# Optimization experiments

Hardware: AMD Instinct MI355X
Metric: run time of the kernel (lower is better)

Reference implementation:

```python
import jax, jax.numpy as jnp
import numpy as np

B, S, D, H = 2, 2048, 2048, 16
HD = D // H  # head_dim = 128


def setup_inputs() -> dict:
    key = jax.random.key(0)
    k1, k2, k3, k4, k5, k6 = jax.random.split(key, 6)
    scale = 1.0 / np.sqrt(D)
    return {
        "hidden_states": jax.random.normal(k1, (B, S, D), dtype=jnp.float32),
        "attention_mask": jnp.ones((B, S), dtype=jnp.int32),
        "wq": jax.random.normal(k2, (D, D), dtype=jnp.float32) * scale,
        "wk": jax.random.normal(k3, (D, D), dtype=jnp.float32) * scale,
        "wv": jax.random.normal(k4, (D, D), dtype=jnp.float32) * scale,
        "wo": jax.random.normal(k5, (D, D), dtype=jnp.float32) * scale,
        "bo": jax.random.normal(k6, (D,), dtype=jnp.float32) * 0.01,
    }


def reference(hidden_states, attention_mask, wq, wk, wv, wo, bo):
    b, s, d = hidden_states.shape
    # QKV projections (no bias), split heads -> [B, S, H, HD]
    q = (hidden_states @ wq).reshape(b, s, H, HD)
    k = (hidden_states @ wk).reshape(b, s, H, HD)
    v = (hidden_states @ wv).reshape(b, s, H, HD)

    # combined causal + padding mask -> [B, 1, S, S]
    causal = jnp.tril(jnp.ones((s, s), dtype=bool))[None, None]
    pad = (attention_mask > 0)[:, None, None, :]  # [B,1,1,S]
    mask = jnp.logical_and(causal, pad)

    big_neg = jnp.finfo(hidden_states.dtype).min
    bias = jnp.where(mask, 0.0, big_neg).astype(hidden_states.dtype)

    # scaled dot-product attention (flax dot_product_attention scales by 1/sqrt(head_dim))
    scores = jnp.einsum("bqhd,bkhd->bhqk", q, k) / jnp.sqrt(jnp.asarray(HD, hidden_states.dtype))
    probs = jax.nn.softmax(scores + bias, axis=-1)
    ctx = jnp.einsum("bhqk,bkhd->bqhd", probs, v).reshape(b, s, d)

    return ctx @ wo + bo
```

## Files before the change

### kernel.cpp

```cpp
#include <hip/hip_runtime.h>
#include <hip/hip_bf16.h>
#include <stdint.h>

#define Bv 2
#define Sv 2048
#define Dv 2048
#define Hv 16
#define HDv 128
#define Mv (Bv*Sv)

typedef __attribute__((ext_vector_type(8))) short short8;
typedef __attribute__((ext_vector_type(4))) short short4v;
typedef __attribute__((ext_vector_type(4))) float f32x4;

__device__ __forceinline__ unsigned short bf16_rne(float f) {
    union { float f; uint32_t u; } c; c.f = f;
    uint32_t u = c.u;
    u += 0x7fffu + ((u >> 16) & 1u);
    return (unsigned short)(u >> 16);
}

__device__ __forceinline__ uint32_t cvt_pk_bf16(float lo, float hi) {
    uint32_t r;
    asm("v_cvt_pk_bf16_f32 %0, %1, %2" : "=v"(r) : "v"(lo), "v"(hi));
    return r;
}

__device__ __forceinline__ void gload16(const void* g, void* l) {
    __builtin_amdgcn_global_load_lds((const __attribute__((address_space(1))) void*)g,
                                     (__attribute__((address_space(3))) void*)l, 16, 0, 0);
}

#define BARRIER() asm volatile("s_barrier" ::: "memory")
#define LGKM0()   do { asm volatile("s_waitcnt lgkmcnt(0)" ::: "memory"); \
                       __builtin_amdgcn_sched_barrier(0); } while (0)

__global__ void cvt_x_kernel(const float* __restrict__ x, unsigned short* __restrict__ xb) {
    int i = (blockIdx.x * 256 + threadIdx.x) * 8;
    float4 v0 = *(const float4*)(x + i);
    float4 v1 = *(const float4*)(x + i + 4);
    short8 o;
    o[0] = (short)bf16_rne(v0.x); o[1] = (short)bf16_rne(v0.y);
    o[2] = (short)bf16_rne(v0.z); o[3] = (short)bf16_rne(v0.w);
    o[4] = (short)bf16_rne(v1.x); o[5] = (short)bf16_rne(v1.y);
    o[6] = (short)bf16_rne(v1.z); o[7] = (short)bf16_rne(v1.w);
    *(short8*)(xb + i) = o;
}

__global__ void cvt_wt_kernel(const float* __restrict__ w0, const float* __restrict__ w1,
                              const float* __restrict__ w2, const float* __restrict__ w3,
                              unsigned short* __restrict__ wt) {
    __shared__ unsigned short t[64 * 65];
    const int tid = threadIdx.x;
    int z = blockIdx.z;
    const float* w = (z == 0) ? w0 : (z == 1) ? w1 : (z == 2) ? w2 : w3;
    unsigned short* o = wt + (size_t)z * Dv * Dv;
    int k0 = blockIdx.x * 64, n0 = blockIdx.y * 64;
    #pragma unroll
    for (int j = 0; j < 4; ++j) {
        int r = (tid >> 4) + j * 16;
        int c = (tid & 15) * 4;
        float4 v = *(const float4*)&w[(size_t)(k0 + r) * Dv + n0 + c];
        t[r * 65 + c + 0] = bf16_rne(v.x);
        t[r * 65 + c + 1] = bf16_rne(v.y);
        t[r * 65 + c + 2] = bf16_rne(v.z);
        t[r * 65 + c + 3] = bf16_rne(v.w);
    }
    __syncthreads();
    #pragma unroll
    for (int j = 0; j < 2; ++j) {
        int flat = tid + j * 256;
        int nn = flat >> 3;
        int kk = (flat & 7) * 8;
        short8 v;
        #pragma unroll
        for (int e = 0; e < 8; ++e) v[e] = (short)t[(kk + e) * 65 + nn];
        *(short8*)&o[(size_t)(n0 + nn) * Dv + k0 + kk] = v;
    }
}

__global__ __launch_bounds__(512, 2) void gemm8ph_kernel(
    const unsigned short* __restrict__ A,
    const unsigned short* __restrict__ WtBase,
    unsigned short* __restrict__ CbBase)
{
    extern __shared__ unsigned short lds[];
    const int tid = threadIdx.x;
    const int wv = tid >> 6, ln = tid & 63;
    const int lr = ln & 15, lg = ln >> 4;
    const int wm = wv >> 2, wn = wv & 3;

    const int bid = blockIdx.x;
    const int xcd = bid & 7, idx = bid >> 3;
    const int n_idx = xcd * 2 + idx / 16;
    const int m_idx = idx % 16;
    const int m0 = m_idx * 256, n0g = n_idx * 256;

    const int lrow = wv * 8 + (ln >> 3);
    const int lcol = ((ln & 7) ^ (ln >> 3)) << 3;
    const unsigned short* Ag = A      + (size_t)(m0  + lrow) * Dv + lcol;
    const unsigned short* Bg = WtBase + (size_t)(n0g + lrow) * Dv + lcol;

    auto SH = [&](int T, int isB, int h) {
        const unsigned short* src = (isB ? Bg : Ag) + (size_t)(h * 128) * Dv + T * 64;
        unsigned short* dst = &lds[(T & 1) * 32768 + isB * 16384 + h * 8192 + wv * 512];
        gload16(src, dst);
        gload16(src + (size_t)64 * Dv, dst + 4096);
    };

    const int axk = lr & 7;
    auto RDA = [&](int buf, int fm, int ks) {
        return *(const short8*)&lds[buf * 32768 + (wm * 128 + fm * 16 + lr) * 64 + (((ks * 4 + lg) ^ axk) << 3)];
    };
    auto RDB = [&](int buf, int fn, int ks) {
        return *(const short8*)&lds[buf * 32768 + 16384 + (wn * 64 + fn * 16 + lr) * 64 + (((ks * 4 + lg) ^ axk) << 3)];
    };

    f32x4 acc[8][4];
    #pragma unroll
    for (int fm = 0; fm < 8; fm++)
        #pragma unroll
        for (int fn = 0; fn < 4; fn++)
            acc[fm][fn] = (f32x4){0.f, 0.f, 0.f, 0.f};

    SH(0, 0, 0); SH(0, 0, 1); SH(0, 1, 0); SH(0, 1, 1);
    SH(1, 1, 0); SH(1, 0, 0);
    asm volatile("s_waitcnt vmcnt(4)" ::: "memory");
    BARRIER();

    short8 af[8], b0[4], b1[4];
    const int NT2 = 16;

    #define MFMA_BLK(FN0, FN1, BARR) do {                                              \
        __builtin_amdgcn_s_setprio(1);                                                 \
        _Pragma("unroll")                                                              \
        for (int fm = 0; fm < 8; fm++) {                                               \
            acc[fm][FN0] = __builtin_amdgcn_mfma_f32_16x16x32_bf16(af[fm], BARR[FN0], acc[fm][FN0], 0, 0, 0); \
            acc[fm][FN1] = __builtin_amdgcn_mfma_f32_16x16x32_bf16(af[fm], BARR[FN1], acc[fm][FN1], 0, 0, 0); \
        }                                                                              \
        __builtin_amdgcn_s_setprio(0);                                                 \
    } while (0)

    for (int i = 0; i < NT2; ++i) {
        const int Tb = 2 * i + 1;
        const bool more = (i + 1 < NT2);

        #pragma unroll
        for (int fm = 0; fm < 8; fm++) af[fm] = RDA(0, fm, 0);
        #pragma unroll
        for (int fn = 0; fn < 4; fn++) b0[fn] = RDB(0, fn, 0);
        SH(Tb, 0, 1);
        BARRIER(); LGKM0();
        MFMA_BLK(0, 1, b0);
        BARRIER();

        #pragma unroll
        for (int fn = 0; fn < 4; fn++) b1[fn] = RDB(0, fn, 1);
        SH(Tb, 1, 1);
        BARRIER(); LGKM0();
        MFMA_BLK(2, 3, b0);
        BARRIER();

        #pragma unroll
        for (int fm = 0; fm < 8; fm++) af[fm] = RDA(0, fm, 1);
        if (more) SH(Tb + 1, 1, 0);
        BARRIER(); LGKM0();
        MFMA_BLK(0, 1, b1);
        BARRIER();

        if (more) SH(Tb + 1, 0, 0);
        BARRIER(); LGKM0();
        MFMA_BLK(2, 3, b1);
        if (more) asm volatile("s_waitcnt vmcnt(4)" ::: "memory");
        else      asm volatile("s_waitcnt vmcnt(0)" ::: "memory");
        BARRIER();

        #pragma unroll
        for (int fm = 0; fm < 8; fm++) af[fm] = RDA(1, fm, 0);
        #pragma unroll
        for (int fn = 0; fn < 4; fn++) b0[fn] = RDB(1, fn, 0);
        if (more) SH(Tb + 1, 0, 1);
        BARRIER(); LGKM0();
        MFMA_BLK(0, 1, b0);
        BARRIER();

        #pragma unroll
        for (int fn = 0; fn < 4; fn++) b1[fn] = RDB(1, fn, 1);
        if (more) SH(Tb + 1, 1, 1);
        BARRIER(); LGKM0();
        MFMA_BLK(2, 3, b0);
        BARRIER();

        #pragma unroll
        for (int fm = 0; fm < 8; fm++) af[fm] = RDA(1, fm, 1);
        if (more) SH(Tb + 2, 1, 0);
        BARRIER(); LGKM0();
        MFMA_BLK(0, 1, b1);
        BARRIER();

        if (more) SH(Tb + 2, 0, 0);
        BARRIER(); LGKM0();
        MFMA_BLK(2, 3, b1);
        if (more) {
            asm volatile("s_waitcnt vmcnt(4)" ::: "memory");
            BARRIER();
        }
    }
    #undef MFMA_BLK

    const int z = n0g >> 11;
    unsigned short* Cz = CbBase + (size_t)z * Mv * Dv;
    const int ncl = (n0g & 2047) + wn * 64;
    #pragma unroll
    for (int fm = 0; fm < 8; fm++)
        #pragma unroll
        for (int fn = 0; fn < 4; fn++) {
            int row = m0 + wm * 128 + fm * 16 + lg * 4;
            int col = ncl + fn * 16 + lr;
            #pragma unroll
            for (int r = 0; r < 4; r++)
                Cz[(size_t)(row + r) * Dv + col] = bf16_rne(acc[fm][fn][r]);
        }
}

template<int FOUT>
__global__ __launch_bounds__(512, 2) void gemm8_kernel(
    const unsigned short* __restrict__ A,
    const unsigned short* __restrict__ WtBase,
    unsigned short* __restrict__ Cb,
    float* __restrict__ Cf,
    const float* __restrict__ bias)
{
    extern __shared__ unsigned short lds[];
    const int tid = threadIdx.x;
    const int wv = tid >> 6, ln = tid & 63;
    const int lr = ln & 15, lg = ln >> 4;
    const int wm = wv >> 2, wn = wv & 3;

    const int bid = blockIdx.x;
    const int xcd = bid & 7, idx = bid >> 3;
    const int n_idx = xcd;
    const int m_idx = idx;
    const int m0 = m_idx * 128;
    const int n0g = n_idx * 256;
    const int NT = Dv / 64;

    const int srow = ln >> 3;
    const int swz = ((ln & 7) ^ srow) << 3;
    const unsigned short* Ab = A      + (size_t)(m0  + wv * 8 + srow) * Dv + swz;
    const unsigned short* Bb = WtBase + (size_t)(n0g + wv * 8 + srow) * Dv + swz;

    auto STAGE_A = [&](int t, int d) {
        const unsigned short* g = Ab + t * 64;
        #pragma unroll
        for (int j = 0; j < 2; ++j)
            gload16(g + (size_t)(j * 64) * Dv, &lds[d * 24576 + (j * 64 + wv * 8) * 64]);
    };
    auto STAGE_B = [&](int t, int d) {
        const unsigned short* g = Bb + t * 64;
        #pragma unroll
        for (int j = 0; j < 4; ++j)
            gload16(g + (size_t)(j * 64) * Dv, &lds[d * 24576 + 8192 + (j * 64 + wv * 8) * 64]);
    };

    const int aro = (wm * 64 + lr) * 64;
    const int bro = (wn * 64 + lr) * 64;
    const int ach0 = ((lg ^ (lr & 7)) << 3);
    const int ach1 = (((4 + lg) ^ (lr & 7)) << 3);

    f32x4 acc[4][4];
    #pragma unroll
    for (int mi = 0; mi < 4; mi++)
        #pragma unroll
        for (int ni = 0; ni < 4; ni++)
            acc[mi][ni] = (f32x4){0.f, 0.f, 0.f, 0.f};

    STAGE_A(0, 0); STAGE_B(0, 0);
    STAGE_A(1, 1); STAGE_B(1, 1);
    asm volatile("s_waitcnt vmcnt(6)" ::: "memory");
    BARRIER();

    for (int t = 0; t < NT; ++t) {
        const int d = t % 3, d2 = (t + 2) % 3;
        const unsigned short* la = &lds[d * 24576];
        const unsigned short* lb = &lds[d * 24576 + 8192];

        short8 af[4][2], bf0[2][2];
        #pragma unroll
        for (int mi = 0; mi < 4; mi++) {
            af[mi][0] = *(const short8*)&la[aro + mi * 1024 + ach0];
            af[mi][1] = *(const short8*)&la[aro + mi * 1024 + ach1];
        }
        #pragma unroll
        for (int ni = 0; ni < 2; ni++) {
            bf0[ni][0] = *(const short8*)&lb[bro + ni * 1024 + ach0];
            bf0[ni][1] = *(const short8*)&lb[bro + ni * 1024 + ach1];
        }
        if (t + 2 < NT) STAGE_A(t + 2, d2);
        BARRIER();
        __builtin_amdgcn_s_setprio(1);
        #pragma unroll
        for (int mi = 0; mi < 4; mi++)
            #pragma unroll
            for (int ni = 0; ni < 2; ni++) {
                acc[mi][ni] = __builtin_amdgcn_mfma_f32_16x16x32_bf16(af[mi][0], bf0[ni][0], acc[mi][ni], 0, 0, 0);
                acc[mi][ni] = __builtin_amdgcn_mfma_f32_16x16x32_bf16(af[mi][1], bf0[ni][1], acc[mi][ni], 0, 0, 0);
            }
        __builtin_amdgcn_s_setprio(0);

        short8 bf1[2][2];
        #pragma unroll
        for (int ni = 0; ni < 2; ni++) {
            bf1[ni][0] = *(const short8*)&lb[bro + (ni + 2) * 1024 + ach0];
            bf1[ni][1] = *(const short8*)&lb[bro + (ni + 2) * 1024 + ach1];
        }
        if (t + 2 < NT) STAGE_B(t + 2, d2);
        asm volatile("s_waitcnt vmcnt(6)" ::: "memory");
        BARRIER();
        __builtin_amdgcn_s_setprio(1);
        #pragma unroll
        for (int mi = 0; mi < 4; mi++)
            #pragma unroll
            for (int ni = 0; ni < 2; ni++) {
                acc[mi][ni + 2] = __builtin_amdgcn_mfma_f32_16x16x32_bf16(af[mi][0], bf1[ni][0], acc[mi][ni + 2], 0, 0, 0);
                acc[mi][ni + 2] = __builtin_amdgcn_mfma_f32_16x16x32_bf16(af[mi][1], bf1[ni][1], acc[mi][ni + 2], 0, 0, 0);
            }
        __builtin_amdgcn_s_setprio(0);
    }

    if (FOUT) {
        #pragma unroll
        for (int mi = 0; mi < 4; mi++)
            #pragma unroll
            for (int ni = 0; ni < 4; ni++) {
                int row = m0 + wm * 64 + mi * 16 + lg * 4;
                int col = n0g + wn * 64 + ni * 16 + lr;
                float bv = bias[col];
                #pragma unroll
                for (int r = 0; r < 4; r++)
                    Cf[(size_t)(row + r) * Dv + col] = acc[mi][ni][r] + bv;
            }
    } else {
        __syncthreads();
        unsigned short* T = lds;
        #pragma unroll
        for (int mi = 0; mi < 4; mi++)
            #pragma unroll
            for (int ni = 0; ni < 4; ni++) {
                int row = wm * 64 + mi * 16 + lg * 4;
                int col = wn * 64 + ni * 16 + lr;
                int cb = (row >> 2) ^ (col & 31);
                short4v o;
                #pragma unroll
                for (int r = 0; r < 4; r++) o[r] = (short)bf16_rne(acc[mi][ni][r]);
                *(short4v*)&T[col * 128 + cb * 4] = o;
            }
        __syncthreads();
        const int bb = m0 >> 11;
        const int s0 = m0 & 2047;
        unsigned short* VTb = Cb + (size_t)bb * Dv * Sv;
        #pragma unroll
        for (int j = 0; j < 8; ++j) {
            int flat = tid + j * 512;
            int col = flat >> 4;
            int s16 = flat & 15;
            int c5 = col & 31;
            short4v lo = *(const short4v*)&T[col * 128 + (((s16 * 2)     ^ c5) << 2)];
            short4v hi = *(const short4v*)&T[col * 128 + (((s16 * 2 + 1) ^ c5) << 2)];
            short8 v;
            v[0] = lo[0]; v[1] = lo[1]; v[2] = lo[2]; v[3] = lo[3];
            v[4] = hi[0]; v[5] = hi[1]; v[6] = hi[2]; v[7] = hi[3];
            *(short8*)&VTb[(size_t)(n0g + col) * Sv + s0 + s16 * 8] = v;
        }
    }
}

__global__ __launch_bounds__(512) void attn_kernel(
    const unsigned short* __restrict__ Q, const unsigned short* __restrict__ K,
    const unsigned short* __restrict__ VT, const int* __restrict__ pmask,
    unsigned short* __restrict__ CTX)
{
    __shared__ unsigned short lK[2][64 * 128];
    __shared__ unsigned short lVt[2][128 * 64];
    __shared__ int lPmB[2][64];
    __shared__ int lPmOk[2];

    const int tid = threadIdx.x, wv = tid >> 6, ln = tid & 63;
    const int lr = ln & 15, lg = ln >> 4;
    const int L = blockIdx.x;
    const int bh = (L & 7) * 4 + ((L >> 3) & 3);
    const int b = bh >> 4, h = bh & 15;
    const int v = L >> 5;
    const int qidx = (v < 8) ? (15 - v) : (v - 8);
    const int q0 = qidx * 128;
    const int qw0 = q0 + wv * 16;
    const size_t hoff  = (size_t)b * Sv * Dv + (size_t)h * HDv;
    const size_t vtoff = ((size_t)b * Dv + (size_t)h * HDv) * Sv;

    short8 qf[4];
    #pragma unroll
    for (int ds = 0; ds < 4; ds++)
        qf[ds] = *(const short8*)&Q[hoff + (size_t)(qw0 + lr) * Dv + ds * 32 + lg * 8];

    size_t koff[2], voff[2];
    #pragma unroll
    for (int ii = 0; ii < 2; ++ii) {
        int slot = ii * 512 + wv * 64 + ln;
        int krow = slot >> 4, kch = slot & 15;
        koff[ii] = hoff + (size_t)krow * Dv + ((kch ^ (krow & 7)) << 3);
        int vrow = slot >> 3, vch = slot & 7;
        voff[ii] = vtoff + (size_t)vrow * Sv + ((vch ^ (vrow & 7)) << 3);
    }

    auto STAGE = [&](int t, int buf) {
        const size_t kadd = (size_t)(t << 6) * Dv;
        const int vadd = t << 6;
        unsigned short* kb = &lK[buf][0];
        unsigned short* vb = &lVt[buf][0];
        #pragma unroll
        for (int ii = 0; ii < 2; ++ii) {
            gload16(K + koff[ii] + kadd, kb + (ii * 512 + wv * 64) * 8);
            gload16(VT + voff[ii] + vadd, vb + (ii * 512 + wv * 64) * 8);
        }
        if (wv == 0) {
            int pmv = pmask[b * Sv + (t << 6) + ln];
            lPmB[buf][ln] = pmv;
            unsigned long long bal = __ballot(pmv != 0);
            if (ln == 0) lPmOk[buf] = (bal == ~0ull) ? 1 : 0;
        }
    };

    f32x4 acc[8];
    #pragma unroll
    for (int n = 0; n < 8; n++) acc[n] = (f32x4){0.f, 0.f, 0.f, 0.f};
    float mrow = -3.0e38f, lrow = 0.f;
    const float CS = 0.12751744f;
    const int qg = qw0 + lr;
    const int nt = (q0 >> 6) + 2;
    const int srcA = lr + ((lg & 1) << 5);
    const int srcB = srcA + 16;
    const bool hiSel = (lg >= 2);

    auto TILE = [&](int t, int buf, auto CAUSAL_c) {
        constexpr bool CAUSAL = decltype(CAUSAL_c)::value;
        const int kv0 = t << 6;
        const unsigned short* kb = &lK[buf][0];
        const unsigned short* vb = &lVt[buf][0];

        f32x4 st[4];
        #pragma unroll
        for (int t2 = 0; t2 < 4; ++t2) st[t2] = (f32x4){0.f, 0.f, 0.f, 0.f};
        __builtin_amdgcn_s_setprio(1);
        #pragma unroll
        for (int t2 = 0; t2 < 4; ++t2) {
            const int krow = t2 * 16 + lr;
            #pragma unroll
            for (int ds = 0; ds < 4; ++ds) {
                const int ch = ds * 4 + lg;
                short8 kf = *(const short8*)&kb[krow * 128 + ((ch ^ (krow & 7)) << 3)];
                st[t2] = __builtin_amdgcn_mfma_f32_16x16x32_bf16(kf, qf[ds], st[t2], 0, 0, 0);
            }
        }
        __builtin_amdgcn_s_setprio(0);

        float sv[4][4];
        float rmax;
        if constexpr (CAUSAL) {
            const int* pm = &lPmB[buf][0];
            #pragma unroll
            for (int t2 = 0; t2 < 4; ++t2)
                #pragma unroll
                for (int r = 0; r < 4; ++r) {
                    int kvl = t2 * 16 + lg * 4 + r;
                    bool ok = ((kv0 + kvl) <= qg) && (pm[kvl] != 0);
                    sv[t2][r] = ok ? st[t2][r] * CS : -1.0e30f;
                }
            rmax = sv[0][0];
            #pragma unroll
            for (int t2 = 0; t2 < 4; ++t2)
                #pragma unroll
                for (int r = 0; r < 4; ++r) rmax = fmaxf(rmax, sv[t2][r]);
            rmax = fmaxf(rmax, __shfl_xor(rmax, 16, 64));
            rmax = fmaxf(rmax, __shfl_xor(rmax, 32, 64));
        } else {
            rmax = st[0][0];
            #pragma unroll
            for (int t2 = 0; t2 < 4; ++t2)
                #pragma unroll
                for (int r = 0; r < 4; ++r) rmax = fmaxf(rmax, st[t2][r]);
            rmax = fmaxf(rmax, __shfl_xor(rmax, 16, 64));
            rmax = fmaxf(rmax, __shfl_xor(rmax, 32, 64));
            rmax *= CS;
        }

        if (!__all(rmax - mrow <= 8.0f)) {
            float mn = fmaxf(mrow, rmax);
            float alpha = exp2f(mrow - mn);
            mrow = mn;
            lrow *= alpha;
            #pragma unroll
            for (int n = 0; n < 8; n++)
                #pragma unroll
                for (int r = 0; r < 4; r++) acc[n][r] *= alpha;
        }

        float p[4][4]; float psum = 0.f;
        if constexpr (CAUSAL) {
            #pragma unroll
            for (int t2 = 0; t2 < 4; ++t2)
                #pragma unroll
                for (int r = 0; r < 4; ++r) {
                    float e = exp2f(sv[t2][r] - mrow);
                    p[t2][r] = (sv[t2][r] > -5.0e29f) ? e : 0.f;
                    psum += p[t2][r];
                }
        } else {
            if (lPmOk[buf]) {
                #pragma unroll
                for (int t2 = 0; t2 < 4; ++t2)
                    #pragma unroll
                    for (int r = 0; r < 4; ++r) {
                        p[t2][r] = exp2f(fmaf(st[t2][r], CS, -mrow));
                        psum += p[t2][r];
                    }
            } else {
                const int* pm = &lPmB[buf][0];
                #pragma unroll
                for (int t2 = 0; t2 < 4; ++t2)
                    #pragma unroll
                    for (int r = 0; r < 4; ++r) {
                        int kvl = t2 * 16 + lg * 4 + r;
                        float e = exp2f(fmaf(st[t2][r], CS, -mrow));
                        p[t2][r] = (pm[kvl] != 0) ? e : 0.f;
                        psum += p[t2][r];
                    }
            }
        }
        psum += __shfl_xor(psum, 16, 64);
        psum += __shfl_xor(psum, 32, 64);
        lrow += psum;

        uint32_t pk[4][2];
        #pragma unroll
        for (int t2 = 0; t2 < 4; ++t2)
            #pragma unroll
            for (int pp = 0; pp < 2; ++pp)
                pk[t2][pp] = cvt_pk_bf16(p[t2][2 * pp], p[t2][2 * pp + 1]);

        union U { uint32_t u[4]; short8 s; } pa0, pa1;
        {
            uint32_t l0 = (uint32_t)__shfl((int)pk[0][0], srcA, 64), h0 = (uint32_t)__shfl((int)pk[1][0], srcA, 64);
            uint32_t l1 = (uint32_t)__shfl((int)pk[0][1], srcA, 64), h1 = (uint32_t)__shfl((int)pk[1][1], srcA, 64);
            uint32_t l2 = (uint32_t)__shfl((int)pk[0][0], srcB, 64), h2 = (uint32_t)__shfl((int)pk[1][0], srcB, 64);
            uint32_t l3 = (uint32_t)__shfl((int)pk[0][1], srcB, 64), h3 = (uint32_t)__shfl((int)pk[1][1], srcB, 64);
            pa0.u[0] = hiSel ? h0 : l0; pa0.u[1] = hiSel ? h1 : l1;
            pa0.u[2] = hiSel ? h2 : l2; pa0.u[3] = hiSel ? h3 : l3;
        }
        {
            uint32_t l0 = (uint32_t)__shfl((int)pk[2][0], srcA, 64), h0 = (uint32_t)__shfl((int)pk[3][0], srcA, 64);
            uint32_t l1 = (uint32_t)__shfl((int)pk[2][1], srcA, 64), h1 = (uint32_t)__shfl((int)pk[3][1], srcA, 64);
            uint32_t l2 = (uint32_t)__shfl((int)pk[2][0], srcB, 64), h2 = (uint32_t)__shfl((int)pk[3][0], srcB, 64);
            uint32_t l3 = (uint32_t)__shfl((int)pk[2][1], srcB, 64), h3 = (uint32_t)__shfl((int)pk[3][1], srcB, 64);
            pa1.u[0] = hiSel ? h0 : l0; pa1.u[1] = hiSel ? h1 : l1;
            pa1.u[2] = hiSel ? h2 : l2; pa1.u[3] = hiSel ? h3 : l3;
        }

        __builtin_amdgcn_s_setprio(1);
        #pragma unroll
        for (int n = 0; n < 8; n++) {
            const int vrow = n * 16 + lr;
            short8 a0 = *(const short8*)&vb[vrow * 64 + ((lg ^ (vrow & 7)) << 3)];
            acc[n] = __builtin_amdgcn_mfma_f32_16x16x32_bf16(a0, pa0.s, acc[n], 0, 0, 0);
            short8 a1 = *(const short8*)&vb[vrow * 64 + (((4 + lg) ^ (vrow & 7)) << 3)];
            acc[n] = __builtin_amdgcn_mfma_f32_16x16x32_bf16(a1, pa1.s, acc[n], 0, 0, 0);
        }
        __builtin_amdgcn_s_setprio(0);
    };

    STAGE(0, 0);
    __syncthreads();
    int cur = 0;

    for (int t = 0; t < nt; ++t) {
        if (t + 1 < nt) STAGE(t + 1, cur ^ 1);
        const int kv0 = t << 6;
        if (kv0 <= qw0 + 15) {
            if (kv0 + 63 > qw0) TILE(t, cur, std::integral_constant<bool, true>{});
            else                TILE(t, cur, std::integral_constant<bool, false>{});
        }
        __syncthreads();
        cur ^= 1;
    }

    float inv = 1.0f / lrow;
    #pragma unroll
    for (int n = 0; n < 8; n++) {
        short4v o;
        #pragma unroll
        for (int r = 0; r < 4; r++) o[r] = (short)bf16_rne(acc[n][r] * inv);
        *(short4v*)&CTX[hoff + (size_t)qg * Dv + n * 16 + lg * 4] = o;
    }
}

extern "C" void kernel_launch(void* const* d_in, const int* in_sizes, int n_in,
                              void* d_out, int out_size, void* d_ws, size_t ws_size,
                              hipStream_t stream) {
    const float* hs  = (const float*)d_in[0];
    const int*   am  = (const int*)d_in[1];
    const float* wq  = (const float*)d_in[2];
    const float* wk  = (const float*)d_in[3];
    const float* wv_ = (const float*)d_in[4];
    const float* wo  = (const float*)d_in[5];
    const float* bo  = (const float*)d_in[6];
    float* out = (float*)d_out;

    char* ws = (char*)d_ws;
    unsigned short* Xb  = (unsigned short*)ws;
    unsigned short* Wt  = (unsigned short*)(ws + (size_t)16 * 1024 * 1024);
    unsigned short* QKV = (unsigned short*)(ws + (size_t)48 * 1024 * 1024);
    unsigned short* CTX = (unsigned short*)(ws + (size_t)96 * 1024 * 1024);
    unsigned short* VT  = QKV + 2 * (size_t)Mv * Dv;

    const int LDSB_8PH = 131072;
    const int LDSB_R   = 147456;
    static bool attrSet = false;
    if (!attrSet) {
        hipFuncSetAttribute((const void*)gemm8ph_kernel, hipFuncAttributeMaxDynamicSharedMemorySize, LDSB_8PH);
        hipFuncSetAttribute((const void*)gemm8_kernel<0>, hipFuncAttributeMaxDynamicSharedMemorySize, LDSB_R);
        hipFuncSetAttribute((const void*)gemm8_kernel<1>, hipFuncAttributeMaxDynamicSharedMemorySize, LDSB_R);
        attrSet = true;
    }

    hipLaunchKernelGGL(cvt_x_kernel, dim3(Mv * Dv / 8 / 256), dim3(256), 0, stream, hs, Xb);
    hipLaunchKernelGGL(cvt_wt_kernel, dim3(32, 32, 4), dim3(256), 0, stream, wq, wk, wv_, wo, Wt);
    hipLaunchKernelGGL(gemm8ph_kernel, dim3(256), dim3(512), LDSB_8PH, stream, Xb, Wt, QKV);
    hipLaunchKernelGGL(gemm8_kernel<0>, dim3(256), dim3(512), LDSB_R, stream,
                       Xb, Wt + 2 * (size_t)Dv * Dv, VT, (float*)nullptr, (const float*)nullptr);
    hipLaunchKernelGGL(attn_kernel, dim3(512), dim3(512), 0, stream,
                       QKV, QKV + (size_t)Mv * Dv, VT, am, CTX);
    hipLaunchKernelGGL(gemm8_kernel<1>, dim3(256), dim3(512), LDSB_R, stream,
                       CTX, Wt + 3 * (size_t)Dv * Dv, (unsigned short*)nullptr, out, bo);
}
```

Before: 227.6 us.

## Split heavy causal query tiles across two KV halves and merge partial results

The eight heaviest causal query tiles per head are each split into two blocks that cover separate halves of the KV range. The grid grows from 512 to 768 blocks, which evens out work per block across the CUs. Each half writes an unnormalized bf16 partial output plus its row max and sum into workspace that reuses the already-consumed Wq/Wk/Wv weight buffers. A new merge kernel then rescales and combines the halves into CTX. The cost is an extra launch, extra global traffic for the partials, and bf16 rounding of the unnormalized partial accumulators.

```diff
diff --git a/kernel.cpp b/kernel.cpp
--- a/kernel.cpp
+++ b/kernel.cpp
@@ -18,6 +18,11 @@
     uint32_t u = c.u;
     u += 0x7fffu + ((u >> 16) & 1u);
     return (unsigned short)(u >> 16);
+}
+
+__device__ __forceinline__ float bf16_to_f(unsigned short s) {
+    union { uint32_t u; float f; } c; c.u = ((uint32_t)s) << 16;
+    return c.f;
 }
 
 __device__ __forceinline__ uint32_t cvt_pk_bf16(float lo, float hi) {
@@ -378,7 +383,8 @@
 __global__ __launch_bounds__(512) void attn_kernel(
     const unsigned short* __restrict__ Q, const unsigned short* __restrict__ K,
     const unsigned short* __restrict__ VT, const int* __restrict__ pmask,
-    unsigned short* __restrict__ CTX)
+    unsigned short* __restrict__ CTX,
+    unsigned short* __restrict__ PO, float* __restrict__ PML)
 {
     __shared__ unsigned short lK[2][64 * 128];
     __shared__ unsigned short lVt[2][128 * 64];
@@ -390,8 +396,22 @@
     const int L = blockIdx.x;
     const int bh = (L & 7) * 4 + ((L >> 3) & 3);
     const int b = bh >> 4, h = bh & 15;
-    const int v = L >> 5;
-    const int qidx = (v < 8) ? (15 - v) : (v - 8);
+    const int s = L >> 5;
+    int qidx, t0, t1, half = 0;
+    bool heavy;
+    if (s < 16) {
+        heavy = true;
+        qidx = 15 - (s >> 1);
+        half = s & 1;
+        int ht = qidx + 1;
+        t0 = half ? ht : 0;
+        t1 = half ? (2 * qidx + 2) : ht;
+    } else {
+        heavy = false;
+        qidx = 23 - s;
+        t0 = 0;
+        t1 = 2 * qidx + 2;
+    }
     const int q0 = qidx * 128;
     const int qw0 = q0 + wv * 16;
     const size_t hoff  = (size_t)b * Sv * Dv + (size_t)h * HDv;
@@ -436,7 +456,6 @@
     float mrow = -3.0e38f, lrow = 0.f;
     const float CS = 0.12751744f;
     const int qg = qw0 + lr;
-    const int nt = (q0 >> 6) + 2;
     const int srcA = lr + ((lg & 1) << 5);
     const int srcB = srcA + 16;
     const bool hiSel = (lg >= 2);
@@ -577,12 +596,12 @@
         __builtin_amdgcn_s_setprio(0);
     };
 
-    STAGE(0, 0);
+    STAGE(t0, 0);
     __syncthreads();
     int cur = 0;
 
-    for (int t = 0; t < nt; ++t) {
-        if (t + 1 < nt) STAGE(t + 1, cur ^ 1);
+    for (int t = t0; t < t1; ++t) {
+        if (t + 1 < t1) STAGE(t + 1, cur ^ 1);
         const int kv0 = t << 6;
         if (kv0 <= qw0 + 15) {
             if (kv0 + 63 > qw0) TILE(t, cur, std::integral_constant<bool, true>{});
@@ -592,13 +611,65 @@
         cur ^= 1;
     }
 
-    float inv = 1.0f / lrow;
-    #pragma unroll
-    for (int n = 0; n < 8; n++) {
-        short4v o;
-        #pragma unroll
-        for (int r = 0; r < 4; r++) o[r] = (short)bf16_rne(acc[n][r] * inv);
-        *(short4v*)&CTX[hoff + (size_t)qg * Dv + n * 16 + lg * 4] = o;
+    if (!heavy) {
+        float inv = 1.0f / lrow;
+        #pragma unroll
+        for (int n = 0; n < 8; n++) {
+            short4v o;
+            #pragma unroll
+            for (int r = 0; r < 4; r++) o[r] = (short)bf16_rne(acc[n][r] * inv);
+            *(short4v*)&CTX[hoff + (size_t)qg * Dv + n * 16 + lg * 4] = o;
+        }
+    } else {
+        const int qtl = qidx - 8;
+        const int ql = qg - q0;
+        const size_t base = ((size_t)(bh * 8 + qtl) * 2 + half) * 128 + ql;
+        #pragma unroll
+        for (int n = 0; n < 8; n++) {
+            short4v o;
+            #pragma unroll
+            for (int r = 0; r < 4; r++) o[r] = (short)bf16_rne(acc[n][r]);
+            *(short4v*)&PO[base * 128 + n * 16 + lg * 4] = o;
+        }
+        if (lg == 0) {
+            PML[base * 2]     = mrow;
+            PML[base * 2 + 1] = lrow;
+        }
+    }
+}
+
+__global__ __launch_bounds__(256) void merge_kernel(
+    const unsigned short* __restrict__ PO, const float* __restrict__ PML,
+    unsigned short* __restrict__ CTX)
+{
+    const int qt = blockIdx.x;
+    const int bh = blockIdx.y;
+    const int b = bh >> 4, h = bh & 15;
+    const size_t hoff = (size_t)b * Sv * Dv + (size_t)h * HDv;
+    const int tid = threadIdx.x;
+    #pragma unroll
+    for (int it = 0; it < 8; ++it) {
+        int idx = tid + it * 256;
+        int row = idx >> 4;
+        int c8  = (idx & 15) * 8;
+        size_t base0 = ((size_t)(bh * 8 + qt) * 2) * 128 + row;
+        size_t base1 = base0 + 128;
+        float mA = PML[base0 * 2], lA = PML[base0 * 2 + 1];
+        float mB = PML[base1 * 2], lB = PML[base1 * 2 + 1];
+        float m = fmaxf(mA, mB);
+        float aA = exp2f(mA - m), aB = exp2f(mB - m);
+        float inv = 1.0f / (lA * aA + lB * aB);
+        short8 oA = *(const short8*)&PO[base0 * 128 + c8];
+        short8 oB = *(const short8*)&PO[base1 * 128 + c8];
+        int q = (qt + 8) * 128 + row;
+        short8 o;
+        #pragma unroll
+        for (int j = 0; j < 8; ++j) {
+            float fa = bf16_to_f((unsigned short)oA[j]);
+            float fb = bf16_to_f((unsigned short)oB[j]);
+            o[j] = (short)bf16_rne((fa * aA + fb * aB) * inv);
+        }
+        *(short8*)&CTX[hoff + (size_t)q * Dv + c8] = o;
     }
 }
 
@@ -620,6 +691,8 @@
     unsigned short* QKV = (unsigned short*)(ws + (size_t)48 * 1024 * 1024);
     unsigned short* CTX = (unsigned short*)(ws + (size_t)96 * 1024 * 1024);
     unsigned short* VT  = QKV + 2 * (size_t)Mv * Dv;
+    unsigned short* PO  = Wt;
+    float*          PML = (float*)(ws + (size_t)32 * 1024 * 1024);
 
     const int LDSB_8PH = 131072;
     const int LDSB_R   = 147456;
@@ -636,8 +709,9 @@
     hipLaunchKernelGGL(gemm8ph_kernel, dim3(256), dim3(512), LDSB_8PH, stream, Xb, Wt, QKV);
     hipLaunchKernelGGL(gemm8_kernel<0>, dim3(256), dim3(512), LDSB_R, stream,
                        Xb, Wt + 2 * (size_t)Dv * Dv, VT, (float*)nullptr, (const float*)nullptr);
-    hipLaunchKernelGGL(attn_kernel, dim3(512), dim3(512), 0, stream,
-                       QKV, QKV + (size_t)Mv * Dv, VT, am, CTX);
+    hipLaunchKernelGGL(attn_kernel, dim3(768), dim3(512), 0, stream,
+                       QKV, QKV + (size_t)Mv * Dv, VT, am, CTX, PO, PML);
+    hipLaunchKernelGGL(merge_kernel, dim3(8, 32), dim3(256), 0, stream, PO, PML, CTX);
     hipLaunchKernelGGL(gemm8_kernel<1>, dim3(256), dim3(512), LDSB_R, stream,
                        CTX, Wt + 3 * (size_t)Dv * Dv, (unsigned short*)nullptr, out, bo);
 }
```

After: 244.9 us. +7.6%, slower.
